# Optimization experiments

Measured on AMD Instinct MI355X. Metric: run time of the kernel, lower is better.

The kernel has to match this reference:

```python
import jax, jax.numpy as jnp
import numpy as np

N_ATOMS = 2048
REPLICATES = 3          # fixed in source
CENTER_CELL = 13        # index of (0,0,0) offset among the 27 images


def setup_inputs() -> dict:
    key = jax.random.key(0)
    k1, k2, k3 = jax.random.split(key, 3)
    # Slightly perturbed cubic lattice, ~30 Angstrom box
    cell = 30.0 * jnp.eye(3, dtype=jnp.float32) + 0.5 * jax.random.normal(k1, (3, 3), dtype=jnp.float32)
    frac = jax.random.uniform(k2, (N_ATOMS, 3), dtype=jnp.float32)
    positions = frac @ cell  # cartesian positions inside the cell
    numbers = jax.random.randint(k3, (N_ATOMS,), 0, 100, dtype=jnp.int64)
    return {"positions": positions, "cell": cell, "numbers": numbers, "k": 12}


def reference(positions, cell, numbers, k):
    N = positions.shape[0]
    dt = positions.dtype
    # --- create_labeled_supercell: 3x3x3 images, offsets in {-1,0,1} ---
    r = jnp.arange(-1, 2)
    offs = jnp.stack(jnp.meshgrid(r, r, r, indexing="ij"), axis=-1).reshape(-1, 3).astype(dt)  # [27,3]
    shift = offs @ cell                                   # [27,3] cartesian shifts
    pos_sc = (positions[None, :, :] + shift[:, None, :]).reshape(-1, 3)  # [27N,3]
    # atom_id = tile(arange(N),27) => global_idx % N ; cell_id = global_idx // N
    # --- box_filter: keep points within central cell expanded by dx ---
    row_norm = jnp.linalg.norm(cell, axis=1)              # [3]
    dx = 0.1 * jnp.min(row_norm)
    frac = pos_sc @ jnp.linalg.inv(cell)                  # fractional coords [27N,3]
    eps = dx / row_norm                                   # margin in fractional units
    valid = jnp.all((frac >= -eps) & (frac <= 1.0 + eps), axis=1)  # [27N]
    # --- KNN for central-cell nodes (== periodic-graph dst nodes) ---
    center = pos_sc[CENTER_CELL * N:(CENTER_CELL + 1) * N]  # [N,3] == positions
    d2 = (jnp.sum(center * center, axis=1)[:, None]
          + jnp.sum(pos_sc * pos_sc, axis=1)[None, :]
          - 2.0 * center @ pos_sc.T)                      # [N, 27N]
    big = jnp.asarray(1e30, dt)
    d2 = jnp.where(valid[None, :], d2, big)               # drop box-filtered nodes
    self_idx = CENTER_CELL * N + jnp.arange(N)
    d2 = d2.at[jnp.arange(N), self_idx].set(big)          # exclude self-loops
    neg_d2, idx = jax.lax.top_k(-d2, k)                   # [N,k] nearest neighbors
    src_pos = pos_sc[idx]                                 # [N,k,3]
    edge_vec = (src_pos - center[:, None, :]).reshape(-1, 3)   # [N*k,3]
    dist = jnp.sqrt(jnp.maximum(-neg_d2, 0.0)).reshape(-1)     # [N*k]
    # --- create_periodic_graph: map src supercell node -> original atom_id ---
    src_atom = (idx % N).reshape(-1)                      # [N*k] int
    dst_atom = jnp.repeat(jnp.arange(N), k)               # [N*k] int
    return edge_vec, dist, src_atom, dst_atom, numbers
```

## Files before the change

kernel.cpp:

```cpp
#include <hip/hip_runtime.h>
#include <stdint.h>

#define N_ATOMS   2048
#define NREP      27
#define NCAND     (NREP * N_ATOMS)
#define KNN       12
#define CAP       128
#define CAPC      8192
#define NEDGE     (N_ATOMS * KNN)
#define OFF_EDGE  0
#define OFF_DIST  (3 * NEDGE)
#define OFF_SRC   (OFF_DIST + NEDGE)
#define OFF_DST   (OFF_SRC + NEDGE)
#define OFF_NUM   (OFF_DST + NEDGE)
#define WS_CAND_OFF 256
#define WS_IDX_OFF  (WS_CAND_OFF + CAPC * 16)

__global__ __launch_bounds__(256) void prep_kernel(
    const float* __restrict__ pos, const float* __restrict__ cell,
    const int* __restrict__ numbers, unsigned* __restrict__ hdr,
    float4* __restrict__ cand, unsigned* __restrict__ cidx,
    float* __restrict__ out)
{
    int m = blockIdx.x * 256 + threadIdx.x;

    float c[9];
#pragma unroll
    for (int q = 0; q < 9; ++q) c[q] = cell[q];

    double a00 = c[0], a01 = c[1], a02 = c[2];
    double a10 = c[3], a11 = c[4], a12 = c[5];
    double a20 = c[6], a21 = c[7], a22 = c[8];
    double det = a00 * (a11 * a22 - a12 * a21)
               - a01 * (a10 * a22 - a12 * a20)
               + a02 * (a10 * a21 - a11 * a20);
    double id = 1.0 / det;
    float M[9];
    M[0] = (float)(( a11 * a22 - a12 * a21) * id);
    M[1] = (float)((-(a01 * a22 - a02 * a21)) * id);
    M[2] = (float)(( a01 * a12 - a02 * a11) * id);
    M[3] = (float)((-(a10 * a22 - a12 * a20)) * id);
    M[4] = (float)(( a00 * a22 - a02 * a20) * id);
    M[5] = (float)((-(a00 * a12 - a02 * a10)) * id);
    M[6] = (float)(( a10 * a21 - a11 * a20) * id);
    M[7] = (float)((-(a00 * a21 - a01 * a20)) * id);
    M[8] = (float)(( a00 * a11 - a01 * a10) * id);

    int j = m >> 11, i = m & (N_ATOMS - 1);
    float o0 = (float)(j / 9 - 1);
    float o1 = (float)((j / 3) % 3 - 1);
    float o2 = (float)(j % 3 - 1);
    float sx = __fadd_rn(__fadd_rn(__fmul_rn(o0, c[0]), __fmul_rn(o1, c[3])), __fmul_rn(o2, c[6]));
    float sy = __fadd_rn(__fadd_rn(__fmul_rn(o0, c[1]), __fmul_rn(o1, c[4])), __fmul_rn(o2, c[7]));
    float sz = __fadd_rn(__fadd_rn(__fmul_rn(o0, c[2]), __fmul_rn(o1, c[5])), __fmul_rn(o2, c[8]));
    float px = __fadd_rn(pos[i * 3 + 0], sx);
    float py = __fadd_rn(pos[i * 3 + 1], sy);
    float pz = __fadd_rn(pos[i * 3 + 2], sz);

    float rn[3];
#pragma unroll
    for (int r = 0; r < 3; ++r)
        rn[r] = sqrtf(c[r*3]*c[r*3] + c[r*3+1]*c[r*3+1] + c[r*3+2]*c[r*3+2]);
    float dx = 0.1f * fminf(rn[0], fminf(rn[1], rn[2]));
    bool valid = true;
#pragma unroll
    for (int d = 0; d < 3; ++d) {
        float f = __fmaf_rn(pz, M[6 + d], __fmaf_rn(py, M[3 + d], __fmul_rn(px, M[d])));
        float eps = dx / rn[d];
        valid = valid && (f >= -eps) && (f <= 1.0f + eps);
    }

    unsigned long long ball = __ballot(valid);
    int lane = threadIdx.x & 63;
    int nv = __popcll(ball);
    unsigned base = 0;
    if (lane == 0 && nv) base = atomicAdd(hdr, (unsigned)nv);
    base = __shfl(base, 0, 64);
    if (valid) {
        unsigned s = base + __popcll(ball & ((1ull << lane) - 1ull));
        if (s < CAPC) {
            float pp = __fadd_rn(__fadd_rn(__fmul_rn(px, px), __fmul_rn(py, py)), __fmul_rn(pz, pz));
            cand[s] = make_float4(px, py, pz, pp);
            cidx[s] = (unsigned)m;
        }
    }

    if (m == 0) {
        float vol = (float)fabs(det);
        float T = powf(3.0f * 48.0f * vol / (4.0f * 3.14159265f * (float)N_ATOMS), 2.0f / 3.0f);
        ((float*)hdr)[1] = T;
    }
    if (m < N_ATOMS) out[OFF_NUM + m] = (float)numbers[m];
}

__global__ __launch_bounds__(256) void knn_kernel(
    const float* __restrict__ pos, const float* __restrict__ cell,
    const unsigned* __restrict__ hdr, const float4* __restrict__ cand,
    const unsigned* __restrict__ cidx, float* __restrict__ out)
{
    __shared__ unsigned long long sh_keys[CAP];
    __shared__ int sh_cnt;

    const int a = blockIdx.x;
    const int tid = threadIdx.x;

    float c[9];
#pragma unroll
    for (int q = 0; q < 9; ++q) c[q] = cell[q];

    const float cx = pos[a * 3 + 0];
    const float cy = pos[a * 3 + 1];
    const float cz = pos[a * 3 + 2];
    const float cc = __fadd_rn(__fadd_rn(__fmul_rn(cx, cx), __fmul_rn(cy, cy)), __fmul_rn(cz, cz));

    const int cnt_c = min((int)hdr[0], CAPC);
    float T = ((const float*)hdr)[1];
    const int self_m = 13 * N_ATOMS + a;
    int cnt = 0;

    for (int att = 0; att < 16; ++att) {
        if (tid == 0) sh_cnt = 0;
        __syncthreads();
        for (int i = tid; i < cnt_c; i += 256) {
            float4 p = cand[i];
            float dot = __fmaf_rn(cz, p.z, __fmaf_rn(cy, p.y, __fmul_rn(cx, p.x)));
            float d2 = __fsub_rn(__fadd_rn(cc, p.w), __fmul_rn(2.0f, dot));
            if (d2 < T) {
                unsigned mi = cidx[i];
                if ((int)mi != self_m) {
                    int slot = atomicAdd(&sh_cnt, 1);
                    if (slot < CAP)
                        sh_keys[slot] = ((unsigned long long)__float_as_uint(d2) << 32) | mi;
                }
            }
        }
        __syncthreads();
        cnt = sh_cnt;
        __syncthreads();
        if (cnt >= KNN && cnt <= CAP) break;
        T = (cnt < KNN) ? T * 2.0f : T * 0.5f;
    }

    if (tid < 64) {
        const unsigned long long MAXK = ~0ull;
        unsigned long long k0 = (tid < cnt) ? sh_keys[tid] : MAXK;
        unsigned long long k1 = (tid + 64 < cnt) ? sh_keys[tid + 64] : MAXK;
        unsigned long long lo = (k0 < k1) ? k0 : k1;
        unsigned long long hi = (k0 < k1) ? k1 : k0;
#pragma unroll
        for (int r = 0; r < KNN; ++r) {
            unsigned long long mn = lo;
#pragma unroll
            for (int off = 32; off; off >>= 1) {
                unsigned long long o = __shfl_xor(mn, off, 64);
                mn = (o < mn) ? o : mn;
            }
            if (lo == mn) { lo = hi; hi = MAXK; }
            if (tid == r) {
                unsigned mm = (unsigned)(mn & 0xffffffffu);
                float d2 = __uint_as_float((unsigned)(mn >> 32));
                int jj = (int)(mm >> 11), ii = (int)(mm & (N_ATOMS - 1));
                float o0 = (float)(jj / 9 - 1);
                float o1 = (float)((jj / 3) % 3 - 1);
                float o2 = (float)(jj % 3 - 1);
                float sx = __fadd_rn(__fadd_rn(__fmul_rn(o0, c[0]), __fmul_rn(o1, c[3])), __fmul_rn(o2, c[6]));
                float sy = __fadd_rn(__fadd_rn(__fmul_rn(o0, c[1]), __fmul_rn(o1, c[4])), __fmul_rn(o2, c[7]));
                float sz = __fadd_rn(__fadd_rn(__fmul_rn(o0, c[2]), __fmul_rn(o1, c[5])), __fmul_rn(o2, c[8]));
                float px = __fadd_rn(pos[ii * 3 + 0], sx);
                float py = __fadd_rn(pos[ii * 3 + 1], sy);
                float pz = __fadd_rn(pos[ii * 3 + 2], sz);
                int e = a * KNN + r;
                out[OFF_EDGE + 3 * e + 0] = __fsub_rn(px, cx);
                out[OFF_EDGE + 3 * e + 1] = __fsub_rn(py, cy);
                out[OFF_EDGE + 3 * e + 2] = __fsub_rn(pz, cz);
                out[OFF_DIST + e] = sqrtf(fmaxf(d2, 0.0f));
                out[OFF_SRC + e]  = (float)(mm & (N_ATOMS - 1));
                out[OFF_DST + e]  = (float)a;
            }
        }
    }
}

extern "C" void kernel_launch(void* const* d_in, const int* in_sizes, int n_in,
                              void* d_out, int out_size, void* d_ws, size_t ws_size,
                              hipStream_t stream) {
    const float* pos     = (const float*)d_in[0];
    const float* cell    = (const float*)d_in[1];
    const int*   numbers = (const int*)d_in[2];
    float*       out     = (float*)d_out;

    unsigned* hdr  = (unsigned*)d_ws;
    float4*   cand = (float4*)((char*)d_ws + WS_CAND_OFF);
    unsigned* cidx = (unsigned*)((char*)d_ws + WS_IDX_OFF);

    hipMemsetAsync(d_ws, 0, 4, stream);

    hipLaunchKernelGGL(prep_kernel, dim3(NCAND / 256), dim3(256), 0, stream,
                       pos, cell, numbers, hdr, cand, cidx, out);
    hipLaunchKernelGGL(knn_kernel, dim3(N_ATOMS), dim3(256), 0, stream,
                       pos, cell, hdr, cand, cidx, out);
}
```

Baseline: 80.65 us.

## Fuse prep and KNN passes into one cooperative kernel with grid sync

Replaces the two-kernel sequence with a single cooperative launch of 1024 blocks. The blocks first build the compacted candidate list, meet at a grid-wide barrier, then each block handles two query atoms in a loop. The search threshold is now recomputed per thread instead of being passed through the workspace header. This removes one kernel launch and the gap between kernels, at the cost of a grid barrier and half as many blocks for the KNN phase. The old two-kernel path stays as a fallback if the cooperative launch fails.

Measured after the change: 203.2 us. +151.9%, slower.

```diff
diff --git a/kernel.cpp b/kernel.cpp
--- a/kernel.cpp
+++ b/kernel.cpp
@@ -1,33 +1,26 @@
 #include <hip/hip_runtime.h>
+#include <hip/hip_cooperative_groups.h>
 #include <stdint.h>
 
-#define N_ATOMS   2048
-#define NREP      27
-#define NCAND     (NREP * N_ATOMS)
-#define KNN       12
-#define CAP       128
-#define CAPC      8192
-#define NEDGE     (N_ATOMS * KNN)
-#define OFF_EDGE  0
-#define OFF_DIST  (3 * NEDGE)
-#define OFF_SRC   (OFF_DIST + NEDGE)
-#define OFF_DST   (OFF_SRC + NEDGE)
-#define OFF_NUM   (OFF_DST + NEDGE)
+namespace cg = cooperative_groups;
+
+#define N_ATOMS 2048
+#define NREP    27
+#define NCAND   (NREP * N_ATOMS)
+#define KNN     12
+#define CAP     128
+#define CAPC    8192
+#define NEDGE   (N_ATOMS * KNN)
+#define COOP_GRID 1024
+#define OFF_EDGE 0
+#define OFF_DIST (3 * NEDGE)
+#define OFF_SRC  (OFF_DIST + NEDGE)
+#define OFF_DST  (OFF_SRC + NEDGE)
+#define OFF_NUM  (OFF_DST + NEDGE)
 #define WS_CAND_OFF 256
 #define WS_IDX_OFF  (WS_CAND_OFF + CAPC * 16)
 
-__global__ __launch_bounds__(256) void prep_kernel(
-    const float* __restrict__ pos, const float* __restrict__ cell,
-    const int* __restrict__ numbers, unsigned* __restrict__ hdr,
-    float4* __restrict__ cand, unsigned* __restrict__ cidx,
-    float* __restrict__ out)
-{
-    int m = blockIdx.x * 256 + threadIdx.x;
-
-    float c[9];
-#pragma unroll
-    for (int q = 0; q < 9; ++q) c[q] = cell[q];
-
+__device__ __forceinline__ void inv_cell(const float* c, float* M) {
     double a00 = c[0], a01 = c[1], a02 = c[2];
     double a10 = c[3], a11 = c[4], a12 = c[5];
     double a20 = c[6], a21 = c[7], a22 = c[8];
@@ -35,7 +28,6 @@
                - a01 * (a10 * a22 - a12 * a20)
                + a02 * (a10 * a21 - a11 * a20);
     double id = 1.0 / det;
-    float M[9];
     M[0] = (float)(( a11 * a22 - a12 * a21) * id);
     M[1] = (float)((-(a01 * a22 - a02 * a21)) * id);
     M[2] = (float)(( a01 * a12 - a02 * a11) * id);
@@ -45,30 +37,179 @@
     M[6] = (float)(( a10 * a21 - a11 * a20) * id);
     M[7] = (float)((-(a00 * a21 - a01 * a20)) * id);
     M[8] = (float)(( a00 * a11 - a01 * a10) * id);
-
-    int j = m >> 11, i = m & (N_ATOMS - 1);
+}
+
+__device__ __forceinline__ bool classify(
+    int g, const float* __restrict__ pos, const float* c, const float* M,
+    float& px, float& py, float& pz)
+{
+    int j = g >> 11, i = g & (N_ATOMS - 1);
     float o0 = (float)(j / 9 - 1);
     float o1 = (float)((j / 3) % 3 - 1);
     float o2 = (float)(j % 3 - 1);
     float sx = __fadd_rn(__fadd_rn(__fmul_rn(o0, c[0]), __fmul_rn(o1, c[3])), __fmul_rn(o2, c[6]));
     float sy = __fadd_rn(__fadd_rn(__fmul_rn(o0, c[1]), __fmul_rn(o1, c[4])), __fmul_rn(o2, c[7]));
     float sz = __fadd_rn(__fadd_rn(__fmul_rn(o0, c[2]), __fmul_rn(o1, c[5])), __fmul_rn(o2, c[8]));
-    float px = __fadd_rn(pos[i * 3 + 0], sx);
-    float py = __fadd_rn(pos[i * 3 + 1], sy);
-    float pz = __fadd_rn(pos[i * 3 + 2], sz);
-
-    float rn[3];
-#pragma unroll
-    for (int r = 0; r < 3; ++r)
-        rn[r] = sqrtf(c[r*3]*c[r*3] + c[r*3+1]*c[r*3+1] + c[r*3+2]*c[r*3+2]);
-    float dx = 0.1f * fminf(rn[0], fminf(rn[1], rn[2]));
-    bool valid = true;
-#pragma unroll
-    for (int d = 0; d < 3; ++d) {
-        float f = __fmaf_rn(pz, M[6 + d], __fmaf_rn(py, M[3 + d], __fmul_rn(px, M[d])));
-        float eps = dx / rn[d];
-        valid = valid && (f >= -eps) && (f <= 1.0f + eps);
-    }
+    px = __fadd_rn(pos[i * 3 + 0], sx);
+    py = __fadd_rn(pos[i * 3 + 1], sy);
+    pz = __fadd_rn(pos[i * 3 + 2], sz);
+    float rn0 = sqrtf(c[0]*c[0] + c[1]*c[1] + c[2]*c[2]);
+    float rn1 = sqrtf(c[3]*c[3] + c[4]*c[4] + c[5]*c[5]);
+    float rn2 = sqrtf(c[6]*c[6] + c[7]*c[7] + c[8]*c[8]);
+    float dxm = 0.1f * fminf(rn0, fminf(rn1, rn2));
+    float f0 = __fmaf_rn(pz, M[6], __fmaf_rn(py, M[3], __fmul_rn(px, M[0])));
+    float f1 = __fmaf_rn(pz, M[7], __fmaf_rn(py, M[4], __fmul_rn(px, M[1])));
+    float f2 = __fmaf_rn(pz, M[8], __fmaf_rn(py, M[5], __fmul_rn(px, M[2])));
+    return (f0 >= -(dxm / rn0)) && (f0 <= 1.0f + dxm / rn0)
+        && (f1 >= -(dxm / rn1)) && (f1 <= 1.0f + dxm / rn1)
+        && (f2 >= -(dxm / rn2)) && (f2 <= 1.0f + dxm / rn2);
+}
+
+__device__ __forceinline__ void emit_edges(
+    int a, int r, unsigned mm, float d2, const float* __restrict__ pos,
+    const float* c, float cx, float cy, float cz, float* __restrict__ out)
+{
+    int jj = (int)(mm >> 11), ii = (int)(mm & (N_ATOMS - 1));
+    float o0 = (float)(jj / 9 - 1);
+    float o1 = (float)((jj / 3) % 3 - 1);
+    float o2 = (float)(jj % 3 - 1);
+    float sx = __fadd_rn(__fadd_rn(__fmul_rn(o0, c[0]), __fmul_rn(o1, c[3])), __fmul_rn(o2, c[6]));
+    float sy = __fadd_rn(__fadd_rn(__fmul_rn(o0, c[1]), __fmul_rn(o1, c[4])), __fmul_rn(o2, c[7]));
+    float sz = __fadd_rn(__fadd_rn(__fmul_rn(o0, c[2]), __fmul_rn(o1, c[5])), __fmul_rn(o2, c[8]));
+    float px = __fadd_rn(pos[ii * 3 + 0], sx);
+    float py = __fadd_rn(pos[ii * 3 + 1], sy);
+    float pz = __fadd_rn(pos[ii * 3 + 2], sz);
+    int e = a * KNN + r;
+    out[OFF_EDGE + 3 * e + 0] = __fsub_rn(px, cx);
+    out[OFF_EDGE + 3 * e + 1] = __fsub_rn(py, cy);
+    out[OFF_EDGE + 3 * e + 2] = __fsub_rn(pz, cz);
+    out[OFF_DIST + e] = sqrtf(fmaxf(d2, 0.0f));
+    out[OFF_SRC + e]  = (float)(mm & (N_ATOMS - 1));
+    out[OFF_DST + e]  = (float)a;
+}
+
+__device__ __forceinline__ float init_T(const float* c) {
+    float vol = fabsf(c[0] * (c[4] * c[8] - c[5] * c[7])
+                    - c[1] * (c[3] * c[8] - c[5] * c[6])
+                    + c[2] * (c[3] * c[7] - c[4] * c[6]));
+    return powf(3.0f * 48.0f * vol / (4.0f * 3.14159265f * (float)N_ATOMS), 2.0f / 3.0f);
+}
+
+__global__ __launch_bounds__(256, 4) void knn_coop(
+    const float* __restrict__ pos, const float* __restrict__ cell,
+    const int* __restrict__ numbers, unsigned* __restrict__ hdr,
+    float4* __restrict__ cand, unsigned* __restrict__ cidx,
+    float* __restrict__ out)
+{
+    __shared__ unsigned long long sh_keys[CAP];
+    __shared__ int sh_cnt;
+
+    const int tid = threadIdx.x;
+    const int g = blockIdx.x * 256 + tid;
+
+    float c[9];
+#pragma unroll
+    for (int q = 0; q < 9; ++q) c[q] = cell[q];
+
+    if (g < NCAND) {
+        float M[9];
+        inv_cell(c, M);
+        float px, py, pz;
+        bool valid = classify(g, pos, c, M, px, py, pz);
+
+        unsigned long long ball = __ballot(valid);
+        int lane = tid & 63;
+        int nv = __popcll(ball);
+        unsigned base = 0;
+        if (lane == 0 && nv) base = atomicAdd(hdr, (unsigned)nv);
+        base = __shfl(base, 0, 64);
+        if (valid) {
+            unsigned s = base + __popcll(ball & ((1ull << lane) - 1ull));
+            if (s < CAPC) {
+                float pp = __fadd_rn(__fadd_rn(__fmul_rn(px, px), __fmul_rn(py, py)), __fmul_rn(pz, pz));
+                cand[s] = make_float4(px, py, pz, pp);
+                cidx[s] = (unsigned)g;
+            }
+        }
+    }
+    if (g < N_ATOMS) out[OFF_NUM + g] = (float)numbers[g];
+
+    cg::this_grid().sync();
+
+    const int cnt_c = min((int)hdr[0], CAPC);
+    const float T0 = init_T(c);
+
+    for (int a = blockIdx.x; a < N_ATOMS; a += COOP_GRID) {
+        const float cx = pos[a * 3 + 0];
+        const float cy = pos[a * 3 + 1];
+        const float cz = pos[a * 3 + 2];
+        const float cc = __fadd_rn(__fadd_rn(__fmul_rn(cx, cx), __fmul_rn(cy, cy)), __fmul_rn(cz, cz));
+        const int self_m = 13 * N_ATOMS + a;
+        float T = T0;
+        int cnt = 0;
+
+        for (int att = 0; att < 16; ++att) {
+            if (tid == 0) sh_cnt = 0;
+            __syncthreads();
+            for (int i = tid; i < cnt_c; i += 256) {
+                float4 p = cand[i];
+                float dot = __fmaf_rn(cz, p.z, __fmaf_rn(cy, p.y, __fmul_rn(cx, p.x)));
+                float d2 = __fsub_rn(__fadd_rn(cc, p.w), __fmul_rn(2.0f, dot));
+                if (d2 < T) {
+                    unsigned mi = cidx[i];
+                    if ((int)mi != self_m) {
+                        int slot = atomicAdd(&sh_cnt, 1);
+                        if (slot < CAP)
+                            sh_keys[slot] = ((unsigned long long)__float_as_uint(d2) << 32) | mi;
+                    }
+                }
+            }
+            __syncthreads();
+            cnt = sh_cnt;
+            __syncthreads();
+            if (cnt >= KNN && cnt <= CAP) break;
+            T = (cnt < KNN) ? T * 2.0f : T * 0.5f;
+        }
+
+        if (tid < 64) {
+            const unsigned long long MAXK = ~0ull;
+            unsigned long long k0 = (tid < cnt) ? sh_keys[tid] : MAXK;
+            unsigned long long k1 = (tid + 64 < cnt) ? sh_keys[tid + 64] : MAXK;
+            unsigned long long lo = (k0 < k1) ? k0 : k1;
+            unsigned long long hi = (k0 < k1) ? k1 : k0;
+#pragma unroll
+            for (int r = 0; r < KNN; ++r) {
+                unsigned long long mn = lo;
+#pragma unroll
+                for (int off = 32; off; off >>= 1) {
+                    unsigned long long o = __shfl_xor(mn, off, 64);
+                    mn = (o < mn) ? o : mn;
+                }
+                if (lo == mn) { lo = hi; hi = MAXK; }
+                if (tid == r)
+                    emit_edges(a, r, (unsigned)(mn & 0xffffffffu),
+                               __uint_as_float((unsigned)(mn >> 32)),
+                               pos, c, cx, cy, cz, out);
+            }
+        }
+        __syncthreads();
+    }
+}
+
+__global__ __launch_bounds__(256) void prep_kernel(
+    const float* __restrict__ pos, const float* __restrict__ cell,
+    const int* __restrict__ numbers, unsigned* __restrict__ hdr,
+    float4* __restrict__ cand, unsigned* __restrict__ cidx,
+    float* __restrict__ out)
+{
+    int m = blockIdx.x * 256 + threadIdx.x;
+    float c[9];
+#pragma unroll
+    for (int q = 0; q < 9; ++q) c[q] = cell[q];
+    float M[9];
+    inv_cell(c, M);
+    float px, py, pz;
+    bool valid = classify(m, pos, c, M, px, py, pz);
 
     unsigned long long ball = __ballot(valid);
     int lane = threadIdx.x & 63;
@@ -84,12 +225,6 @@
             cidx[s] = (unsigned)m;
         }
     }
-
-    if (m == 0) {
-        float vol = (float)fabs(det);
-        float T = powf(3.0f * 48.0f * vol / (4.0f * 3.14159265f * (float)N_ATOMS), 2.0f / 3.0f);
-        ((float*)hdr)[1] = T;
-    }
     if (m < N_ATOMS) out[OFF_NUM + m] = (float)numbers[m];
 }
 
@@ -114,7 +249,7 @@
     const float cc = __fadd_rn(__fadd_rn(__fmul_rn(cx, cx), __fmul_rn(cy, cy)), __fmul_rn(cz, cz));
 
     const int cnt_c = min((int)hdr[0], CAPC);
-    float T = ((const float*)hdr)[1];
+    float T = init_T(c);
     const int self_m = 13 * N_ATOMS + a;
     int cnt = 0;
 
@@ -156,27 +291,10 @@
                 mn = (o < mn) ? o : mn;
             }
             if (lo == mn) { lo = hi; hi = MAXK; }
-            if (tid == r) {
-                unsigned mm = (unsigned)(mn & 0xffffffffu);
-                float d2 = __uint_as_float((unsigned)(mn >> 32));
-                int jj = (int)(mm >> 11), ii = (int)(mm & (N_ATOMS - 1));
-                float o0 = (float)(jj / 9 - 1);
-                float o1 = (float)((jj / 3) % 3 - 1);
-                float o2 = (float)(jj % 3 - 1);
-                float sx = __fadd_rn(__fadd_rn(__fmul_rn(o0, c[0]), __fmul_rn(o1, c[3])), __fmul_rn(o2, c[6]));
-                float sy = __fadd_rn(__fadd_rn(__fmul_rn(o0, c[1]), __fmul_rn(o1, c[4])), __fmul_rn(o2, c[7]));
-                float sz = __fadd_rn(__fadd_rn(__fmul_rn(o0, c[2]), __fmul_rn(o1, c[5])), __fmul_rn(o2, c[8]));
-                float px = __fadd_rn(pos[ii * 3 + 0], sx);
-                float py = __fadd_rn(pos[ii * 3 + 1], sy);
-                float pz = __fadd_rn(pos[ii * 3 + 2], sz);
-                int e = a * KNN + r;
-                out[OFF_EDGE + 3 * e + 0] = __fsub_rn(px, cx);
-                out[OFF_EDGE + 3 * e + 1] = __fsub_rn(py, cy);
-                out[OFF_EDGE + 3 * e + 2] = __fsub_rn(pz, cz);
-                out[OFF_DIST + e] = sqrtf(fmaxf(d2, 0.0f));
-                out[OFF_SRC + e]  = (float)(mm & (N_ATOMS - 1));
-                out[OFF_DST + e]  = (float)a;
-            }
+            if (tid == r)
+                emit_edges(a, r, (unsigned)(mn & 0xffffffffu),
+                           __uint_as_float((unsigned)(mn >> 32)),
+                           pos, c, cx, cy, cz, out);
         }
     }
 }
@@ -195,8 +313,14 @@
 
     hipMemsetAsync(d_ws, 0, 4, stream);
 
-    hipLaunchKernelGGL(prep_kernel, dim3(NCAND / 256), dim3(256), 0, stream,
-                       pos, cell, numbers, hdr, cand, cidx, out);
-    hipLaunchKernelGGL(knn_kernel, dim3(N_ATOMS), dim3(256), 0, stream,
-                       pos, cell, hdr, cand, cidx, out);
-}
+    void* args[] = { (void*)&pos, (void*)&cell, (void*)&numbers,
+                     (void*)&hdr, (void*)&cand, (void*)&cidx, (void*)&out };
+    hipError_t e = hipLaunchCooperativeKernel((void*)knn_coop, dim3(COOP_GRID),
+                                              dim3(256), args, 0, stream);
+    if (e != hipSuccess) {
+        hipLaunchKernelGGL(prep_kernel, dim3(NCAND / 256), dim3(256), 0, stream,
+                           pos, cell, numbers, hdr, cand, cidx, out);
+        hipLaunchKernelGGL(knn_kernel, dim3(N_ATOMS), dim3(256), 0, stream,
+                           pos, cell, hdr, cand, cidx, out);
+    }
+}
```
